# Optimization experiments

Measured on AMD Instinct MI355X. Metric: run time of the kernel, lower is better.

## Reference

```python
import jax, jax.numpy as jnp
import numpy as np

B, S, D, H, BS, L, FF, V = 2, 4096, 1024, 16, 64, 4, 4096, 50000
HD = D // H; NB = S // BS; NM = NB - 2; R = 3

def layernorm(x, g, b):
    mu = x.mean(-1, keepdims=True)
    var = ((x - mu) ** 2).mean(-1, keepdims=True)
    return (x - mu) * jax.lax.rsqrt(var + 1e-5) * g + b

def bigbird_attn(x, neg, rand_attn, Wq, bq, Wk, bk, Wv, bv, Wo, bo):
    heads = lambda t: t.reshape(B, S, H, HD).transpose(0, 2, 1, 3)
    q, k, v = heads(x @ Wq + bq), heads(x @ Wk + bk), heads(x @ Wv + bv)
    scale = np.float32(1.0 / np.sqrt(HD))
    qb = q.reshape(B, H, NB, BS, HD); kb = k.reshape(B, H, NB, BS, HD); vb = v.reshape(B, H, NB, BS, HD)
    negb = neg.reshape(B, NB, BS)
    # global query blocks (first & last) attend densely to all keys
    qg = jnp.concatenate([qb[:, :, 0], qb[:, :, -1]], axis=2)  # [B,H,2*BS,HD]
    sg = jnp.einsum('bhqd,bhkd->bhqk', qg, k) * scale + neg[:, None, None, :]
    ctx_g = jnp.einsum('bhqk,bhkd->bhqd', jax.nn.softmax(sg, -1), v)
    # middle query blocks: sliding window(3) + global(2) + random(R) key blocks
    win_k = jnp.stack([kb[:, :, i:i + NM] for i in range(3)], axis=3)  # [B,H,NM,3,BS,HD]
    win_v = jnp.stack([vb[:, :, i:i + NM] for i in range(3)], axis=3)
    gidx = jnp.array([0, NB - 1])
    g_k = jnp.broadcast_to(kb[:, :, gidx][:, :, None], (B, H, NM, 2, BS, HD))
    g_v = jnp.broadcast_to(vb[:, :, gidx][:, :, None], (B, H, NM, 2, BS, HD))
    hix = jnp.arange(H)[:, None, None]
    r_k = kb[:, hix, rand_attn]  # [B,H,NM,R,BS,HD]
    r_v = vb[:, hix, rand_attn]
    K = 3 + 2 + R
    keys = jnp.concatenate([win_k, g_k, r_k], axis=3).reshape(B, H, NM, K * BS, HD)
    vals = jnp.concatenate([win_v, g_v, r_v], axis=3).reshape(B, H, NM, K * BS, HD)
    win_m = jnp.stack([negb[:, i:i + NM] for i in range(3)], axis=2)  # [B,NM,3,BS]
    g_m = jnp.broadcast_to(negb[:, gidx][:, None], (B, NM, 2, BS))
    m_wg = jnp.concatenate([win_m, g_m], axis=2).reshape(B, 1, NM, 5 * BS)
    r_m = negb[:, rand_attn].reshape(B, H, NM, R * BS)
    m_all = jnp.concatenate([jnp.broadcast_to(m_wg, (B, H, NM, 5 * BS)), r_m], axis=-1)
    sm = jnp.einsum('bhnqd,bhnkd->bhnqk', qb[:, :, 1:-1], keys) * scale + m_all[:, :, :, None, :]
    ctx_m = jnp.einsum('bhnqk,bhnkd->bhnqd', jax.nn.softmax(sm, -1), vals)
    ctx = jnp.concatenate([ctx_g[:, :, None, :BS], ctx_m, ctx_g[:, :, None, BS:]], axis=2)
    out = ctx.reshape(B, H, S, HD).transpose(0, 2, 1, 3).reshape(B, S, D)
    return out @ Wo + bo

def reference(input_ids, attention_mask, rand_attn, emb, Wq, bq, Wk, bk, Wv, bv, Wo, bo, ln1_g, ln1_b, W1, b1, W2, b2, ln2_g, ln2_b, lnf_g, lnf_b, projW, projb):
    x = emb[input_ids]
    neg = (1.0 - attention_mask.astype(jnp.float32)) * (-1e9)
    for l in range(L):  # pre-norm transformer encoder layers
        x = x + bigbird_attn(layernorm(x, ln1_g[l], ln1_b[l]), neg, rand_attn,
                             Wq[l], bq[l], Wk[l], bk[l], Wv[l], bv[l], Wo[l], bo[l])
        h = layernorm(x, ln2_g[l], ln2_b[l])
        x = x + (jax.nn.gelu(h @ W1[l] + b1[l]) @ W2[l] + b2[l])
    x = layernorm(x, lnf_g, lnf_b)
    feats = x.mean(axis=1)  # pooled output (mean over tokens)
    feats = feats / jnp.maximum(jnp.linalg.norm(feats, axis=-1, keepdims=True), 1e-12)
    return feats @ projW + projb

def setup_inputs():
    key = jax.random.key(0)
    ks = jax.random.split(key, 16)
    init = lambda k, shp: (0.02 * jax.random.normal(k, shp)).astype(jnp.float32)
    return {
        'input_ids': jax.random.randint(ks[0], (B, S), 0, V),
        'attention_mask': jnp.ones((B, S), dtype=jnp.int32),
        'rand_attn': jax.random.randint(ks[1], (H, NM, R), 1, NB - 1),
        'emb': init(ks[2], (V, D)),
        'Wq': init(ks[3], (L, D, D)), 'bq': jnp.zeros((L, D), jnp.float32),
        'Wk': init(ks[4], (L, D, D)), 'bk': jnp.zeros((L, D), jnp.float32),
        'Wv': init(ks[5], (L, D, D)), 'bv': jnp.zeros((L, D), jnp.float32),
        'Wo': init(ks[6], (L, D, D)), 'bo': jnp.zeros((L, D), jnp.float32),
        'ln1_g': jnp.ones((L, D), jnp.float32), 'ln1_b': jnp.zeros((L, D), jnp.float32),
        'W1': init(ks[7], (L, D, FF)), 'b1': jnp.zeros((L, FF), jnp.float32),
        'W2': init(ks[8], (L, FF, D)), 'b2': jnp.zeros((L, D), jnp.float32),
        'ln2_g': jnp.ones((L, D), jnp.float32), 'ln2_b': jnp.zeros((L, D), jnp.float32),
        'lnf_g': jnp.ones((D,), jnp.float32), 'lnf_b': jnp.zeros((D,), jnp.float32),
        'projW': init(ks[9], (D, 512)), 'projb': jnp.zeros((512,), jnp.float32),
    }
```

## Files before the change

kernel.cpp:

```cpp
#include <hip/hip_runtime.h>
#include <hip/hip_bf16.h>
#include <cstdint>
#include <cstddef>

#define BATCH 2
#define SEQ   4096
#define DIM   1024
#define NHEAD 16
#define HDIM  64
#define NBLK  64
#define NMID  62
#define NRAND 3
#define NLAYER 4
#define FFDIM 4096
#define ROWS  (BATCH*SEQ)
#define KSPL  8
#define QKVLD (3*DIM)

using f32x4 = __attribute__((ext_vector_type(4))) float;
using s16x8 = __attribute__((ext_vector_type(8))) short;
using s16x4 = __attribute__((ext_vector_type(4))) short;

__device__ inline float bf2f(short s) {
    unsigned u = ((unsigned)(unsigned short)s) << 16;
    union { unsigned u; float f; } cv; cv.u = u; return cv.f;
}
__device__ inline short f2bf(float f) {
    union { float f; unsigned u; } cv; cv.f = f;
    unsigned u = cv.u;
    unsigned r = (u + 0x7fffu + ((u >> 16) & 1u)) >> 16;
    return (short)r;
}
__device__ inline float gelu_f(float x) {
    float u = 0.7978845608028654f * (x + 0.044715f * x * x * x);
    float a = fabsf(u);
    float th = 1.f - 2.f / (1.f + __expf(2.f * a));
    th = copysignf(th, u);
    return 0.5f * x * (1.f + th);
}

__device__ inline void gload16(const short* g, short* l) {
    __builtin_amdgcn_global_load_lds(
        (const __attribute__((address_space(1))) void*)g,
        (__attribute__((address_space(3))) void*)l,
        16, 0, 0);
}

__global__ __launch_bounds__(256) void embed_kernel(
    const int* __restrict__ ids, const float* __restrict__ emb, float* __restrict__ x)
{
    int row = blockIdx.x;
    int id  = ids[row];
    ((float4*)x)[(size_t)row * 256 + threadIdx.x] =
        ((const float4*)emb)[(size_t)id * 256 + threadIdx.x];
}

__global__ __launch_bounds__(256) void neg_kernel(
    const int* __restrict__ mask, float* __restrict__ neg)
{
    int i = blockIdx.x * 256 + threadIdx.x;
    if (i < ROWS) neg[i] = (1.f - (float)mask[i]) * -1e9f;
}

__global__ __launch_bounds__(256) void biaspack_kernel(
    const float* __restrict__ bq, const float* __restrict__ bk,
    const float* __restrict__ bv, float* __restrict__ b3)
{
    int i = blockIdx.x * 256 + threadIdx.x;
    float v = (i < DIM) ? bq[i] : (i < 2 * DIM) ? bk[i - DIM] : bv[i - 2 * DIM];
    b3[i] = v;
}

template<int OUTBF>
__global__ __launch_bounds__(256) void ln_kernel(
    const float* __restrict__ x, const float* __restrict__ g,
    const float* __restrict__ bia, void* __restrict__ out)
{
    __shared__ float s1[4], s2[4];
    int row = blockIdx.x, t = threadIdx.x;
    const float* xr = x + (size_t)row * DIM;
    float4 v = ((const float4*)xr)[t];
    float s = v.x + v.y + v.z + v.w;
    #pragma unroll
    for (int o = 32; o > 0; o >>= 1) s += __shfl_xor(s, o, 64);
    if ((t & 63) == 0) s1[t >> 6] = s;
    __syncthreads();
    float mu = (s1[0] + s1[1] + s1[2] + s1[3]) * (1.f / DIM);
    float dx = v.x - mu, dy = v.y - mu, dz = v.z - mu, dw = v.w - mu;
    float q = dx*dx + dy*dy + dz*dz + dw*dw;
    #pragma unroll
    for (int o = 32; o > 0; o >>= 1) q += __shfl_xor(q, o, 64);
    if ((t & 63) == 0) s2[t >> 6] = q;
    __syncthreads();
    float var = (s2[0] + s2[1] + s2[2] + s2[3]) * (1.f / DIM);
    float rs  = rsqrtf(var + 1e-5f);
    float4 gg = ((const float4*)g)[t];
    float4 bb = ((const float4*)bia)[t];
    float o0 = dx * rs * gg.x + bb.x;
    float o1 = dy * rs * gg.y + bb.y;
    float o2 = dz * rs * gg.z + bb.z;
    float o3 = dw * rs * gg.w + bb.w;
    if (OUTBF) {
        s16x4 ov = { f2bf(o0), f2bf(o1), f2bf(o2), f2bf(o3) };
        ((s16x4*)out)[(size_t)row * (DIM/4) + t] = ov;
    } else {
        float4 ov = { o0, o1, o2, o3 };
        ((float4*)out)[(size_t)row * (DIM/4) + t] = ov;
    }
}

__global__ __launch_bounds__(256) void wconv_kernel(
    const float* __restrict__ W, short* __restrict__ Wt, int K, int N)
{
    __shared__ float tile[32][33];
    int k0 = blockIdx.x * 32, n0 = blockIdx.y * 32;
    int t = threadIdx.x;
    int r = t >> 3, c = (t & 7) * 4;
    float4 v = *(const float4*)(W + (size_t)(k0 + r) * N + n0 + c);
    tile[r][c+0] = v.x; tile[r][c+1] = v.y; tile[r][c+2] = v.z; tile[r][c+3] = v.w;
    __syncthreads();
    s16x4 ov;
    #pragma unroll
    for (int jj = 0; jj < 4; ++jj) ov[jj] = f2bf(tile[c + jj][r]);
    *(s16x4*)(Wt + (size_t)(n0 + r) * K + k0 + c) = ov;
}

__global__ __launch_bounds__(256) void vtrans_kernel(
    const short* __restrict__ qkv, short* __restrict__ vT)
{
    __shared__ short tile[64][66];
    const int sb = blockIdx.x, h = blockIdx.y, b = blockIdx.z;
    const int t = threadIdx.x;
    {
        int row = t >> 2, c0 = (t & 3) * 16;
        const short* src = qkv + 2 * DIM + (size_t)(b * SEQ + sb * 64 + row) * QKVLD + h * HDIM + c0;
        s16x8 a0 = ((const s16x8*)src)[0];
        s16x8 a1 = ((const s16x8*)src)[1];
        #pragma unroll
        for (int i = 0; i < 8; ++i) { tile[row][c0 + i] = a0[i]; tile[row][c0 + 8 + i] = a1[i]; }
    }
    __syncthreads();
    {
        int d = t >> 2, k0 = (t & 3) * 16;
        s16x8 o0, o1;
        #pragma unroll
        for (int i = 0; i < 8; ++i) { o0[i] = tile[k0 + i][d]; o1[i] = tile[k0 + 8 + i][d]; }
        short* dst = vT + (size_t)((b * NHEAD + h) * HDIM + d) * SEQ + sb * 64 + k0;
        ((s16x8*)dst)[0] = o0;
        ((s16x8*)dst)[1] = o1;
    }
}

template<int EPI>
__global__ __launch_bounds__(512) void gemm256_kernel(
    const short* __restrict__ A, const short* __restrict__ Bt,
    const float* __restrict__ bias, const float* __restrict__ resid,
    void* __restrict__ Cout, int M, int N, int K, int klen)
{
    __shared__ short As[2][256 * 64];
    __shared__ short Bs[2][256 * 64];
    const int t = threadIdx.x;
    const int m0 = blockIdx.x * 256, n0 = blockIdx.y * 256;
    const int lane = t & 63, wave = t >> 6;
    const int wm = wave >> 2, wn = wave & 3;
    const int lrow = lane >> 3;
    const int lksw = ((lane & 7) ^ lrow) * 8;

    f32x4 acc[8][4];
    #pragma unroll
    for (int m = 0; m < 8; ++m)
        #pragma unroll
        for (int n = 0; n < 4; ++n)
            acc[m][n] = f32x4{0.f, 0.f, 0.f, 0.f};

    auto STAGE = [&](int side, int kt) {
        #pragma unroll
        for (int c = 0; c < 4; ++c) {
            int chunk = wave + c * 8;
            int row = chunk * 8 + lrow;
            gload16(A  + (size_t)(m0 + row) * K + kt + lksw, &As[side][chunk * 512]);
            gload16(Bt + (size_t)(n0 + row) * K + kt + lksw, &Bs[side][chunk * 512]);
        }
    };

    const int k0 = blockIdx.z * klen;
    STAGE(0, k0);
    __syncthreads();

    int cur = 0;
    for (int kt = k0; kt < k0 + klen; kt += 64) {
        if (kt + 64 < k0 + klen) STAGE(cur ^ 1, kt + 64);
        const short* Ac = As[cur];
        const short* Bc = Bs[cur];
        #pragma unroll
        for (int kk = 0; kk < 2; ++kk) {
            const int cb = kk * 64 + (lane >> 4) * 16;
            s16x8 bfr[4];
            #pragma unroll
            for (int n = 0; n < 4; ++n) {
                int rB = wn * 64 + n * 16 + (lane & 15);
                bfr[n] = *(const s16x8*)((const char*)Bc + rB * 128 + (cb ^ ((rB & 7) << 4)));
            }
            #pragma unroll
            for (int mq = 0; mq < 4; ++mq) {
                s16x8 af[2];
                #pragma unroll
                for (int i = 0; i < 2; ++i) {
                    int rA = wm * 128 + mq * 32 + i * 16 + (lane & 15);
                    af[i] = *(const s16x8*)((const char*)Ac + rA * 128 + (cb ^ ((rA & 7) << 4)));
                }
                #pragma unroll
                for (int i = 0; i < 2; ++i)
                    #pragma unroll
                    for (int n = 0; n < 4; ++n)
                        acc[mq * 2 + i][n] = __builtin_amdgcn_mfma_f32_16x16x32_bf16(
                            af[i], bfr[n], acc[mq * 2 + i][n], 0, 0, 0);
            }
        }
        __syncthreads();
        cur ^= 1;
    }

    const int rbase = m0 + wm * 128 + ((lane >> 4) << 2);
    const int cbase = n0 + wn * 64 + (lane & 15);
    #pragma unroll
    for (int m = 0; m < 8; ++m) {
        #pragma unroll
        for (int n = 0; n < 4; ++n) {
            #pragma unroll
            for (int j = 0; j < 4; ++j) {
                int row = rbase + m * 16 + j;
                int col = cbase + n * 16;
                size_t idx = (size_t)row * N + col;
                float val = acc[m][n][j];
                if (EPI == 3) {
                    ((float*)Cout)[(size_t)blockIdx.z * ((size_t)M * N) + idx] = val;
                } else {
                    val += bias[col];
                    if (EPI == 1) val = gelu_f(val);
                    ((short*)Cout)[idx] = f2bf(val);
                }
            }
        }
    }
    (void)resid;
}

template<int EPI>
__global__ __launch_bounds__(256) void gemm_kernel(
    const short* __restrict__ A, const short* __restrict__ Bt,
    const float* __restrict__ bias, const float* __restrict__ resid,
    void* __restrict__ Cout, int M, int N, int K, int klen)
{
    __shared__ short As[128 * 64];
    __shared__ short Bs[128 * 64];
    const int t = threadIdx.x;
    const int m0 = blockIdx.x * 128, n0 = blockIdx.y * 128;
    const int lane = t & 63, wave = t >> 6;
    const int wr = (wave >> 1) * 64, wc = (wave & 1) * 64;
    const int lrow = lane >> 3;
    const int lksw = ((lane & 7) ^ lrow) * 8;

    f32x4 acc[4][4];
    #pragma unroll
    for (int m = 0; m < 4; ++m)
        #pragma unroll
        for (int n = 0; n < 4; ++n)
            acc[m][n] = f32x4{0.f, 0.f, 0.f, 0.f};

    const int k0 = blockIdx.z * klen;
    for (int kt = k0; kt < k0 + klen; kt += 64) {
        #pragma unroll
        for (int c = 0; c < 4; ++c) {
            int chunk = wave * 4 + c;
            int row = chunk * 8 + lrow;
            gload16(A  + (size_t)(m0 + row) * K + kt + lksw, As + chunk * 512);
            gload16(Bt + (size_t)(n0 + row) * K + kt + lksw, Bs + chunk * 512);
        }
        asm volatile("s_waitcnt vmcnt(0)" ::: "memory");
        __syncthreads();
        #pragma unroll
        for (int kk = 0; kk < 2; ++kk) {
            s16x8 af[4], bfr[4];
            int cb = kk * 64 + (lane >> 4) * 16;
            #pragma unroll
            for (int i = 0; i < 4; ++i) {
                int rA = wr + i * 16 + (lane & 15);
                af[i]  = *(const s16x8*)((const char*)As + rA * 128 + (cb ^ ((rA & 7) << 4)));
                int rB = wc + i * 16 + (lane & 15);
                bfr[i] = *(const s16x8*)((const char*)Bs + rB * 128 + (cb ^ ((rB & 7) << 4)));
            }
            #pragma unroll
            for (int m = 0; m < 4; ++m)
                #pragma unroll
                for (int n = 0; n < 4; ++n)
                    acc[m][n] = __builtin_amdgcn_mfma_f32_16x16x32_bf16(
                        af[m], bfr[n], acc[m][n], 0, 0, 0);
        }
        __syncthreads();
    }

    const int rbase = m0 + wr + ((lane >> 4) << 2);
    const int cbase = n0 + wc + (lane & 15);
    #pragma unroll
    for (int m = 0; m < 4; ++m) {
        #pragma unroll
        for (int n = 0; n < 4; ++n) {
            #pragma unroll
            for (int j = 0; j < 4; ++j) {
                int row = rbase + m * 16 + j;
                int col = cbase + n * 16;
                size_t idx = (size_t)row * N + col;
                float val = acc[m][n][j] + bias[col];
                if (EPI == 1) val = gelu_f(val);
                if (EPI == 2) ((float*)Cout)[idx] = val + resid[idx];
                else          ((short*)Cout)[idx] = f2bf(val);
            }
        }
    }
}

__global__ __launch_bounds__(256) void kred_kernel(
    const float* __restrict__ part, const float* __restrict__ bias, float* __restrict__ x)
{
    const size_t MN = (size_t)ROWS * DIM;
    size_t idx = (size_t)blockIdx.x * DIM + threadIdx.x * 4;
    float4 p0 = *(const float4*)(part + idx);
    float4 p1 = *(const float4*)(part + MN + idx);
    float4 bb = *(const float4*)(bias + threadIdx.x * 4);
    float4 xv = *(const float4*)(x + idx);
    float4 o = { xv.x + p0.x + p1.x + bb.x,
                 xv.y + p0.y + p1.y + bb.y,
                 xv.z + p0.z + p1.z + bb.z,
                 xv.w + p0.w + p1.w + bb.w };
    *(float4*)(x + idx) = o;
}

__device__ inline void attn_tile_mfma(
    const short* __restrict__ kglob, const short* __restrict__ vtglob,
    const float* __restrict__ negp, int kld,
    short* Ks, short* Vs, float* kmask,
    const s16x8* qfrag, f32x4* o, float& mr, float& lsum)
{
    const int t = threadIdx.x;
    const int lane = t & 63;
    const int q15 = lane & 15, g = lane >> 4;
    const int sw = (lane & 7) << 4;

    {
        int row = t >> 2, c0 = (t & 3) * 16;
        int rsw = (row & 7) << 4;
        const short* ksrc = kglob + (size_t)row * kld + c0;
        s16x8 a0 = ((const s16x8*)ksrc)[0];
        s16x8 a1 = ((const s16x8*)ksrc)[1];
        char* kdst = (char*)Ks + row * 128;
        *(s16x8*)(kdst + ((c0 * 2)      ^ rsw)) = a0;
        *(s16x8*)(kdst + ((c0 * 2 + 16) ^ rsw)) = a1;
        const short* vsrc = vtglob + (size_t)row * SEQ + c0;
        s16x8 b0 = ((const s16x8*)vsrc)[0];
        s16x8 b1 = ((const s16x8*)vsrc)[1];
        char* vdst = (char*)Vs + row * 128;
        *(s16x8*)(vdst + ((c0 * 2)      ^ rsw)) = b0;
        *(s16x8*)(vdst + ((c0 * 2 + 16) ^ rsw)) = b1;
        if (t < 16) ((float4*)kmask)[t] = ((const float4*)negp)[t];
    }
    __syncthreads();

    f32x4 s[4];
    #pragma unroll
    for (int f = 0; f < 4; ++f) s[f] = f32x4{0.f, 0.f, 0.f, 0.f};
    #pragma unroll
    for (int ch = 0; ch < 2; ++ch) {
        #pragma unroll
        for (int f = 0; f < 4; ++f) {
            s16x8 kf = *(const s16x8*)((const char*)Ks + (16 * f + q15) * 128 + ((ch * 64 + g * 16) ^ sw));
            s[f] = __builtin_amdgcn_mfma_f32_16x16x32_bf16(kf, qfrag[ch], s[f], 0, 0, 0);
        }
    }

    float p[4][4];
    float mt = -1e30f;
    #pragma unroll
    for (int f = 0; f < 4; ++f) {
        float4 km = ((const float4*)kmask)[f * 4 + g];
        #pragma unroll
        for (int j = 0; j < 4; ++j) {
            float val = s[f][j] * 0.125f + ((const float*)&km)[j];
            p[f][j] = val;
            mt = fmaxf(mt, val);
        }
    }
    mt = fmaxf(mt, __shfl_xor(mt, 16, 64));
    mt = fmaxf(mt, __shfl_xor(mt, 32, 64));
    float mn = fmaxf(mr, mt);
    float psum = 0.f;
    #pragma unroll
    for (int f = 0; f < 4; ++f)
        #pragma unroll
        for (int j = 0; j < 4; ++j) {
            float e = __expf(p[f][j] - mn);
            p[f][j] = e;
            psum += e;
        }
    psum += __shfl_xor(psum, 16, 64);
    psum += __shfl_xor(psum, 32, 64);
    float fc = __expf(mr - mn);
    mr = mn;
    lsum = lsum * fc + psum;
    #pragma unroll
    for (int dt = 0; dt < 4; ++dt)
        #pragma unroll
        for (int j = 0; j < 4; ++j) o[dt][j] *= fc;

    unsigned pk[4][2];
    #pragma unroll
    for (int f = 0; f < 4; ++f)
        #pragma unroll
        for (int pp = 0; pp < 2; ++pp)
            pk[f][pp] = ((unsigned)(unsigned short)f2bf(p[f][2 * pp + 1]) << 16)
                      |  (unsigned)(unsigned short)f2bf(p[f][2 * pp]);

    const int bsel = (lane >> 4) & 1, asel = (lane >> 5) & 1;
    #pragma unroll
    for (int c = 0; c < 2; ++c) {
        union { s16x8 v; int u[4]; } pb;
        #pragma unroll
        for (int w = 0; w < 4; ++w) {
            int src = q15 + 16 * (2 * bsel + (w >> 1));
            int lo = __shfl((int)pk[2 * c][w & 1], src, 64);
            int hi = __shfl((int)pk[2 * c + 1][w & 1], src, 64);
            pb.u[w] = asel ? hi : lo;
        }
        #pragma unroll
        for (int dt = 0; dt < 4; ++dt) {
            s16x8 vf = *(const s16x8*)((const char*)Vs + (16 * dt + q15) * 128 + ((c * 64 + g * 16) ^ sw));
            o[dt] = __builtin_amdgcn_mfma_f32_16x16x32_bf16(vf, pb.v, o[dt], 0, 0, 0);
        }
    }
    __syncthreads();
}

__device__ inline void stage_q64_swz(const short* __restrict__ qglob, int qld, short* Qs)
{
    int t = threadIdx.x;
    int row = t >> 2, c0 = (t & 3) * 16;
    int rsw = (row & 7) << 4;
    const short* src = qglob + (size_t)row * qld + c0;
    s16x8 a0 = ((const s16x8*)src)[0];
    s16x8 a1 = ((const s16x8*)src)[1];
    char* dst = (char*)Qs + row * 128;
    *(s16x8*)(dst + ((c0 * 2)      ^ rsw)) = a0;
    *(s16x8*)(dst + ((c0 * 2 + 16) ^ rsw)) = a1;
}

__global__ __launch_bounds__(256) void attn_middle_mfma(
    const short* __restrict__ qkv, const short* __restrict__ vT,
    const float* __restrict__ neg, const int* __restrict__ rand_attn, short* __restrict__ ctx)
{
    __shared__ short Qs[64 * 64];
    __shared__ short Ks[64 * 64];
    __shared__ short Vs[64 * 64];
    __shared__ float kmask[64];

    const int j = blockIdx.x, h = blockIdx.y, b = blockIdx.z;
    const int n = j + 1;
    const int t = threadIdx.x;
    const int lane = t & 63, wave = t >> 6;
    const int q15 = lane & 15, g = lane >> 4;
    const int sw = (lane & 7) << 4;

    stage_q64_swz(qkv + (size_t)(b * SEQ + n * 64) * QKVLD + h * HDIM, QKVLD, Qs);
    __syncthreads();

    s16x8 qfrag[2];
    {
        int qrow = wave * 16 + q15;
        #pragma unroll
        for (int ch = 0; ch < 2; ++ch)
            qfrag[ch] = *(const s16x8*)((const char*)Qs + qrow * 128 + ((ch * 64 + g * 16) ^ sw));
    }

    int kbl[8];
    kbl[0] = n - 1; kbl[1] = n; kbl[2] = n + 1; kbl[3] = 0; kbl[4] = NBLK - 1;
    {
        const int* ra = rand_attn + ((size_t)h * NMID + j) * NRAND;
        kbl[5] = ra[0]; kbl[6] = ra[1]; kbl[7] = ra[2];
    }

    f32x4 o[4];
    #pragma unroll
    for (int dt = 0; dt < 4; ++dt) o[dt] = f32x4{0.f, 0.f, 0.f, 0.f};
    float mr = -1e30f, lsum = 0.f;

    const short* kbase  = qkv + DIM + (size_t)b * SEQ * QKVLD + h * HDIM;
    const short* vtbase = vT + (size_t)(b * NHEAD + h) * HDIM * SEQ;
    const float* negb   = neg + (size_t)b * SEQ;

    #pragma unroll 1
    for (int ib = 0; ib < 8; ++ib) {
        int kbn = kbl[ib];
        attn_tile_mfma(kbase + (size_t)kbn * 64 * QKVLD, vtbase + kbn * 64,
                       negb + kbn * 64, QKVLD, Ks, Vs, kmask, qfrag, o, mr, lsum);
    }

    float inv = 1.f / lsum;
    short* obase = ctx + (size_t)(b * SEQ + n * 64 + wave * 16 + q15) * DIM + h * HDIM;
    #pragma unroll
    for (int dt = 0; dt < 4; ++dt) {
        s16x4 ov;
        #pragma unroll
        for (int jj = 0; jj < 4; ++jj) ov[jj] = f2bf(o[dt][jj] * inv);
        *(s16x4*)(obase + dt * 16 + g * 4) = ov;
    }
}

__global__ __launch_bounds__(256) void attn_global_mfma(
    const short* __restrict__ qkv, const short* __restrict__ vT,
    const float* __restrict__ neg, float* __restrict__ part)
{
    __shared__ short Qs[64 * 64];
    __shared__ short Ks[64 * 64];
    __shared__ short Vs[64 * 64];
    __shared__ float kmask[64];

    const int qb = blockIdx.x >> 3, ks = blockIdx.x & 7;
    const int h = blockIdx.y, b = blockIdx.z;
    const int tok0 = qb ? (SEQ - 64) : 0;
    const int t = threadIdx.x;
    const int lane = t & 63, wave = t >> 6;
    const int q15 = lane & 15, g = lane >> 4;
    const int sw = (lane & 7) << 4;

    stage_q64_swz(qkv + (size_t)(b * SEQ + tok0) * QKVLD + h * HDIM, QKVLD, Qs);
    __syncthreads();

    s16x8 qfrag[2];
    {
        int qrow = wave * 16 + q15;
        #pragma unroll
        for (int ch = 0; ch < 2; ++ch)
            qfrag[ch] = *(const s16x8*)((const char*)Qs + qrow * 128 + ((ch * 64 + g * 16) ^ sw));
    }

    f32x4 o[4];
    #pragma unroll
    for (int dt = 0; dt < 4; ++dt) o[dt] = f32x4{0.f, 0.f, 0.f, 0.f};
    float mr = -1e30f, lsum = 0.f;

    const short* kbase  = qkv + DIM + (size_t)b * SEQ * QKVLD + h * HDIM;
    const short* vtbase = vT + (size_t)(b * NHEAD + h) * HDIM * SEQ;
    const float* negb   = neg + (size_t)b * SEQ;

    #pragma unroll 1
    for (int ib = 0; ib < 8; ++ib) {
        int kbn = ks * 8 + ib;
        attn_tile_mfma(kbase + (size_t)kbn * 64 * QKVLD, vtbase + kbn * 64,
                       negb + kbn * 64, QKVLD, Ks, Vs, kmask, qfrag, o, mr, lsum);
    }

    float* pbase = part + ((size_t)(((b * NHEAD + h) * 2 + qb) * KSPL + ks)) * 4224;
    int qrow = wave * 16 + q15;
    #pragma unroll
    for (int dt = 0; dt < 4; ++dt)
        *(f32x4*)(pbase + qrow * 64 + dt * 16 + g * 4) = o[dt];
    if (g == 0) { pbase[4096 + qrow] = mr; pbase[4160 + qrow] = lsum; }
}

__global__ __launch_bounds__(256) void attn_greduce(
    const float* __restrict__ part, short* __restrict__ ctx)
{
    const int qb = blockIdx.x, h = blockIdx.y, b = blockIdx.z;
    const int tok0 = qb ? (SEQ - 64) : 0;
    const int t = threadIdx.x;
    const int qq = t >> 2, d0 = (t & 3) * 16;
    const float* base = part + ((size_t)(((b * NHEAD + h) * 2 + qb) * KSPL)) * 4224;

    float m = -1e30f;
    #pragma unroll 1
    for (int s = 0; s < KSPL; ++s)
        m = fmaxf(m, base[(size_t)s * 4224 + 4096 + qq]);
    float L = 0.f;
    float acc[16];
    #pragma unroll
    for (int i = 0; i < 16; ++i) acc[i] = 0.f;
    #pragma unroll 1
    for (int s = 0; s < KSPL; ++s) {
        const float* bp = base + (size_t)s * 4224;
        float w = __expf(bp[4096 + qq] - m);
        L += w * bp[4160 + qq];
        const float4* row = (const float4*)(bp + qq * 64 + d0);
        #pragma unroll
        for (int v4 = 0; v4 < 4; ++v4) {
            float4 val = row[v4];
            acc[v4 * 4 + 0] = fmaf(w, val.x, acc[v4 * 4 + 0]);
            acc[v4 * 4 + 1] = fmaf(w, val.y, acc[v4 * 4 + 1]);
            acc[v4 * 4 + 2] = fmaf(w, val.z, acc[v4 * 4 + 2]);
            acc[v4 * 4 + 3] = fmaf(w, val.w, acc[v4 * 4 + 3]);
        }
    }
    float inv = 1.f / L;
    short* dst = ctx + (size_t)(b * SEQ + tok0 + qq) * DIM + h * HDIM + d0;
    s16x8 o0, o1;
    #pragma unroll
    for (int i = 0; i < 8; ++i) { o0[i] = f2bf(acc[i] * inv); o1[i] = f2bf(acc[8 + i] * inv); }
    ((s16x8*)dst)[0] = o0;
    ((s16x8*)dst)[1] = o1;
}

__global__ __launch_bounds__(256) void colsum1_kernel(
    const float* __restrict__ xln, float* __restrict__ partial)
{
    const int ch = blockIdx.x, b = blockIdx.y, t = threadIdx.x;
    const float* base = xln + ((size_t)b * SEQ + ch * 32) * DIM + t * 4;
    float4 acc = {0.f, 0.f, 0.f, 0.f};
    #pragma unroll 4
    for (int r = 0; r < 32; ++r) {
        float4 v = *(const float4*)(base + (size_t)r * DIM);
        acc.x += v.x; acc.y += v.y; acc.z += v.z; acc.w += v.w;
    }
    *(float4*)(partial + ((size_t)(b * 128 + ch)) * DIM + t * 4) = acc;
}

__global__ __launch_bounds__(256) void colsum2_kernel(
    const float* __restrict__ partial, float* __restrict__ feats)
{
    const int b = blockIdx.x, t = threadIdx.x;
    float4 acc = {0.f, 0.f, 0.f, 0.f};
    #pragma unroll 1
    for (int ch = 0; ch < 128; ++ch) {
        float4 v = *(const float4*)(partial + ((size_t)(b * 128 + ch)) * DIM + t * 4);
        acc.x += v.x; acc.y += v.y; acc.z += v.z; acc.w += v.w;
    }
    const float is = 1.f / SEQ;
    float4 o = { acc.x * is, acc.y * is, acc.z * is, acc.w * is };
    *(float4*)(feats + (size_t)b * DIM + t * 4) = o;
}

__global__ __launch_bounds__(256) void head_kernel(
    const float* __restrict__ feats, const float* __restrict__ projW,
    const float* __restrict__ projb, float* __restrict__ out)
{
    __shared__ float f[DIM];
    __shared__ float slots[4];
    int b = blockIdx.x, t = threadIdx.x;
    float ss = 0.f;
    for (int i = t; i < DIM; i += 256) {
        float vv = feats[b * DIM + i];
        f[i] = vv;
        ss += vv * vv;
    }
    #pragma unroll
    for (int o = 32; o > 0; o >>= 1) ss += __shfl_xor(ss, o, 64);
    if ((t & 63) == 0) slots[t >> 6] = ss;
    __syncthreads();
    float nrm = sqrtf(slots[0] + slots[1] + slots[2] + slots[3]);
    float inv = 1.f / fmaxf(nrm, 1e-12f);
    for (int o = t; o < 512; o += 256) {
        float acc = 0.f;
        for (int d = 0; d < DIM; ++d)
            acc = fmaf(f[d], projW[(size_t)d * 512 + o], acc);
        out[b * 512 + o] = acc * inv + projb[o];
    }
}

extern "C" void kernel_launch(void* const* d_in, const int* in_sizes, int n_in,
                              void* d_out, int out_size, void* d_ws, size_t ws_size,
                              hipStream_t stream)
{
    (void)in_sizes; (void)n_in; (void)out_size; (void)ws_size;
    const int*   ids   = (const int*)d_in[0];
    const int*   amask = (const int*)d_in[1];
    const int*   rnd   = (const int*)d_in[2];
    const float* emb   = (const float*)d_in[3];
    const float* Wq    = (const float*)d_in[4];
    const float* bq    = (const float*)d_in[5];
    const float* Wk    = (const float*)d_in[6];
    const float* bk    = (const float*)d_in[7];
    const float* Wv    = (const float*)d_in[8];
    const float* bv    = (const float*)d_in[9];
    const float* Wo    = (const float*)d_in[10];
    const float* bo    = (const float*)d_in[11];
    const float* ln1g  = (const float*)d_in[12];
    const float* ln1b  = (const float*)d_in[13];
    const float* W1    = (const float*)d_in[14];
    const float* b1    = (const float*)d_in[15];
    const float* W2    = (const float*)d_in[16];
    const float* b2    = (const float*)d_in[17];
    const float* ln2g  = (const float*)d_in[18];
    const float* ln2b  = (const float*)d_in[19];
    const float* lnfg  = (const float*)d_in[20];
    const float* lnfb  = (const float*)d_in[21];
    const float* projW = (const float*)d_in[22];
    const float* projb = (const float*)d_in[23];
    float* out = (float*)d_out;

    char* ws = (char*)d_ws;
    size_t off = 0;
    float* x    = (float*)(ws + off); off += (size_t)ROWS * DIM * 4;
    float* xn_f = (float*)(ws + off);
    short* xn_b = (short*)(ws + off); off += (size_t)ROWS * DIM * 4;
    short* qkv  = (short*)(ws + off); off += (size_t)ROWS * QKVLD * 2;
    short* vT   = (short*)(ws + off); off += (size_t)ROWS * DIM * 2;
    short* ctxb = (short*)(ws + off); off += (size_t)ROWS * DIM * 2;
    short* ffb  = (short*)(ws + off); off += (size_t)ROWS * FFDIM * 2;
    short* wt   = (short*)(ws + off); off += (size_t)FFDIM * DIM * 2;
    float* neg  = (float*)(ws + off); off += (size_t)ROWS * 4;
    float* bias3= (float*)(ws + off); off += (size_t)QKVLD * 4;
    float* feats= (float*)(ws + off); off += (size_t)BATCH * DIM * 4;
    float* part = (float*)(ws + off); off += (size_t)BATCH * NHEAD * 2 * KSPL * 4224 * 4;
    float* cpart= (float*)(ws + off); off += (size_t)BATCH * 128 * DIM * 4;
    float* ff2p = (float*)qkv;

    embed_kernel<<<ROWS, 256, 0, stream>>>(ids, emb, x);
    neg_kernel<<<(ROWS + 255) / 256, 256, 0, stream>>>(amask, neg);

    for (int l = 0; l < NLAYER; ++l) {
        ln_kernel<1><<<ROWS, 256, 0, stream>>>(x, ln1g + l * DIM, ln1b + l * DIM, xn_b);

        wconv_kernel<<<dim3(DIM/32, DIM/32), 256, 0, stream>>>(Wq + (size_t)l*DIM*DIM, wt,               DIM, DIM);
        wconv_kernel<<<dim3(DIM/32, DIM/32), 256, 0, stream>>>(Wk + (size_t)l*DIM*DIM, wt + 1024*1024,   DIM, DIM);
        wconv_kernel<<<dim3(DIM/32, DIM/32), 256, 0, stream>>>(Wv + (size_t)l*DIM*DIM, wt + 2*1024*1024, DIM, DIM);
        biaspack_kernel<<<QKVLD/256, 256, 0, stream>>>(bq + l*DIM, bk + l*DIM, bv + l*DIM, bias3);
        gemm256_kernel<0><<<dim3(ROWS/256, QKVLD/256), 512, 0, stream>>>(xn_b, wt, bias3, nullptr, qkv, ROWS, QKVLD, DIM, DIM);

        vtrans_kernel<<<dim3(SEQ/64, NHEAD, BATCH), 256, 0, stream>>>(qkv, vT);

        attn_global_mfma<<<dim3(2 * KSPL, NHEAD, BATCH), 256, 0, stream>>>(qkv, vT, neg, part);
        attn_middle_mfma<<<dim3(NMID, NHEAD, BATCH), 256, 0, stream>>>(qkv, vT, neg, rnd, ctxb);
        attn_greduce<<<dim3(2, NHEAD, BATCH), 256, 0, stream>>>(part, ctxb);

        wconv_kernel<<<dim3(DIM/32, DIM/32), 256, 0, stream>>>(Wo + (size_t)l*DIM*DIM, wt, DIM, DIM);
        gemm_kernel<2><<<dim3(ROWS/128, DIM/128), 256, 0, stream>>>(ctxb, wt, bo + l*DIM, x, x, ROWS, DIM, DIM, DIM);

        ln_kernel<1><<<ROWS, 256, 0, stream>>>(x, ln2g + l * DIM, ln2b + l * DIM, xn_b);

        wconv_kernel<<<dim3(DIM/32, FFDIM/32), 256, 0, stream>>>(W1 + (size_t)l*DIM*FFDIM, wt, DIM, FFDIM);
        gemm256_kernel<1><<<dim3(ROWS/256, FFDIM/256), 512, 0, stream>>>(xn_b, wt, b1 + l*FFDIM, nullptr, ffb, ROWS, FFDIM, DIM, DIM);
        wconv_kernel<<<dim3(FFDIM/32, DIM/32), 256, 0, stream>>>(W2 + (size_t)l*FFDIM*DIM, wt, FFDIM, DIM);
        gemm256_kernel<3><<<dim3(ROWS/256, DIM/256, 2), 512, 0, stream>>>(ffb, wt, nullptr, nullptr, ff2p, ROWS, DIM, FFDIM, FFDIM/2);
        kred_kernel<<<ROWS, 256, 0, stream>>>(ff2p, b2 + l*DIM, x);
    }

    ln_kernel<0><<<ROWS, 256, 0, stream>>>(x, lnfg, lnfb, xn_f);
    colsum1_kernel<<<dim3(SEQ/32, BATCH), 256, 0, stream>>>(xn_f, cpart);
    colsum2_kernel<<<BATCH, 256, 0, stream>>>(cpart, feats);
    head_kernel<<<BATCH, 256, 0, stream>>>(feats, projW, projb, out);
}
```

Measured before the change: 1.774 ms.

## Restructure 256x256 GEMM main loop into four barrier-separated MFMA phases with split staging

The 256-tile GEMM main loop is rewritten into four quadrant phases. Each phase reads A/B fragments from LDS, then issues the A or B global prefetch for the next k-tile, then runs MFMAs under raised s_setprio between raw s_barriers. The staging layout is changed so each wave loads the rows it will later consume, and an explicit vmcnt wait replaces the end-of-iteration syncthreads. Separately, all weight conversions are hoisted out of the layer loop into per-layer buffers, which uses more workspace but removes the per-layer serialization of conversion kernels. The barrier choreography risks stalls or hazards if the ordering is subtly wrong.

```diff
diff --git a/kernel.cpp b/kernel.cpp
--- a/kernel.cpp
+++ b/kernel.cpp
@@ -16,6 +16,7 @@
 #define ROWS  (BATCH*SEQ)
 #define KSPL  8
 #define QKVLD (3*DIM)
+#define WLAYER (12*1024*1024)
 
 using f32x4 = __attribute__((ext_vector_type(4))) float;
 using s16x8 = __attribute__((ext_vector_type(8))) short;
@@ -163,8 +164,11 @@
     const int m0 = blockIdx.x * 256, n0 = blockIdx.y * 256;
     const int lane = t & 63, wave = t >> 6;
     const int wm = wave >> 2, wn = wave & 3;
+    const int l15 = lane & 15;
     const int lrow = lane >> 3;
     const int lksw = ((lane & 7) ^ lrow) * 8;
+    const int ga = wn;
+    const int hb = wn >> 1, gb = wm * 2 + (wn & 1);
 
     f32x4 acc[8][4];
     #pragma unroll
@@ -173,56 +177,110 @@
         for (int n = 0; n < 4; ++n)
             acc[m][n] = f32x4{0.f, 0.f, 0.f, 0.f};
 
-    auto STAGE = [&](int side, int kt) {
+    auto STAGE_A = [&](int side, int kt) {
         #pragma unroll
         for (int c = 0; c < 4; ++c) {
-            int chunk = wave + c * 8;
-            int row = chunk * 8 + lrow;
-            gload16(A  + (size_t)(m0 + row) * K + kt + lksw, &As[side][chunk * 512]);
-            gload16(Bt + (size_t)(n0 + row) * K + kt + lksw, &Bs[side][chunk * 512]);
+            int row = wm * 128 + c * 32 + ga * 8 + lrow;
+            gload16(A + (size_t)(m0 + row) * K + kt + lksw,
+                    &As[side][wm * 8192 + c * 2048 + ga * 512]);
         }
     };
-
-    const int k0 = blockIdx.z * klen;
-    STAGE(0, k0);
+    auto STAGE_B = [&](int side, int kt) {
+        #pragma unroll
+        for (int c = 0; c < 4; ++c) {
+            int row = hb * 128 + c * 32 + gb * 8 + lrow;
+            gload16(Bt + (size_t)(n0 + row) * K + kt + lksw,
+                    &Bs[side][hb * 8192 + c * 2048 + gb * 512]);
+        }
+    };
+    auto RD_A = [&](const short* buf, int mf, int kk) -> s16x8 {
+        int r = wm * 128 + mf * 16 + l15;
+        int cb = kk * 64 + (lane >> 4) * 16;
+        return *(const s16x8*)((const char*)buf + r * 128 + (cb ^ ((r & 7) << 4)));
+    };
+    auto RD_B = [&](const short* buf, int nf, int kk) -> s16x8 {
+        int r = wn * 64 + nf * 16 + l15;
+        int cb = kk * 64 + (lane >> 4) * 16;
+        return *(const s16x8*)((const char*)buf + r * 128 + (cb ^ ((r & 7) << 4)));
+    };
+
+    const int k0 = blockIdx.z * klen, kend = k0 + klen;
+    STAGE_A(0, k0);
+    STAGE_B(0, k0);
+    asm volatile("s_waitcnt vmcnt(0)" ::: "memory");
     __syncthreads();
 
     int cur = 0;
-    for (int kt = k0; kt < k0 + klen; kt += 64) {
-        if (kt + 64 < k0 + klen) STAGE(cur ^ 1, kt + 64);
+    for (int kt = k0; kt < kend; kt += 64) {
         const short* Ac = As[cur];
         const short* Bc = Bs[cur];
-        #pragma unroll
-        for (int kk = 0; kk < 2; ++kk) {
-            const int cb = kk * 64 + (lane >> 4) * 16;
-            s16x8 bfr[4];
+        const bool nxt = (kt + 64 < kend);
+        s16x8 af[4][2], bf[2][2], bf2[2][2];
+
+        #pragma unroll
+        for (int mf = 0; mf < 4; ++mf) { af[mf][0] = RD_A(Ac, mf, 0); af[mf][1] = RD_A(Ac, mf, 1); }
+        #pragma unroll
+        for (int nf = 0; nf < 2; ++nf) { bf[nf][0] = RD_B(Bc, nf, 0); bf[nf][1] = RD_B(Bc, nf, 1); }
+        if (nxt) STAGE_A(cur ^ 1, kt + 64);
+        __builtin_amdgcn_s_barrier();
+        __builtin_amdgcn_s_setprio(1);
+        #pragma unroll
+        for (int kk = 0; kk < 2; ++kk)
             #pragma unroll
-            for (int n = 0; n < 4; ++n) {
-                int rB = wn * 64 + n * 16 + (lane & 15);
-                bfr[n] = *(const s16x8*)((const char*)Bc + rB * 128 + (cb ^ ((rB & 7) << 4)));
-            }
+            for (int mf = 0; mf < 4; ++mf)
+                #pragma unroll
+                for (int nf = 0; nf < 2; ++nf)
+                    acc[mf][nf] = __builtin_amdgcn_mfma_f32_16x16x32_bf16(af[mf][kk], bf[nf][kk], acc[mf][nf], 0, 0, 0);
+        __builtin_amdgcn_s_setprio(0);
+        __builtin_amdgcn_s_barrier();
+
+        #pragma unroll
+        for (int nf = 0; nf < 2; ++nf) { bf2[nf][0] = RD_B(Bc, 2 + nf, 0); bf2[nf][1] = RD_B(Bc, 2 + nf, 1); }
+        if (nxt) STAGE_B(cur ^ 1, kt + 64);
+        __builtin_amdgcn_s_barrier();
+        __builtin_amdgcn_s_setprio(1);
+        #pragma unroll
+        for (int kk = 0; kk < 2; ++kk)
             #pragma unroll
-            for (int mq = 0; mq < 4; ++mq) {
-                s16x8 af[2];
+            for (int mf = 0; mf < 4; ++mf)
                 #pragma unroll
-                for (int i = 0; i < 2; ++i) {
-                    int rA = wm * 128 + mq * 32 + i * 16 + (lane & 15);
-                    af[i] = *(const s16x8*)((const char*)Ac + rA * 128 + (cb ^ ((rA & 7) << 4)));
-                }
+                for (int nf = 0; nf < 2; ++nf)
+                    acc[mf][2 + nf] = __builtin_amdgcn_mfma_f32_16x16x32_bf16(af[mf][kk], bf2[nf][kk], acc[mf][2 + nf], 0, 0, 0);
+        __builtin_amdgcn_s_setprio(0);
+        __builtin_amdgcn_s_barrier();
+
+        #pragma unroll
+        for (int mf = 0; mf < 4; ++mf) { af[mf][0] = RD_A(Ac, 4 + mf, 0); af[mf][1] = RD_A(Ac, 4 + mf, 1); }
+        __builtin_amdgcn_s_barrier();
+        __builtin_amdgcn_s_setprio(1);
+        #pragma unroll
+        for (int kk = 0; kk < 2; ++kk)
+            #pragma unroll
+            for (int mf = 0; mf < 4; ++mf)
                 #pragma unroll
-                for (int i = 0; i < 2; ++i)
-                    #pragma unroll
-                    for (int n = 0; n < 4; ++n)
-                        acc[mq * 2 + i][n] = __builtin_amdgcn_mfma_f32_16x16x32_bf16(
-                            af[i], bfr[n], acc[mq * 2 + i][n], 0, 0, 0);
-            }
-        }
-        __syncthreads();
+                for (int nf = 0; nf < 2; ++nf)
+                    acc[4 + mf][nf] = __builtin_amdgcn_mfma_f32_16x16x32_bf16(af[mf][kk], bf[nf][kk], acc[4 + mf][nf], 0, 0, 0);
+        __builtin_amdgcn_s_setprio(0);
+        __builtin_amdgcn_s_barrier();
+
+        asm volatile("s_waitcnt vmcnt(0)" ::: "memory");
+        __builtin_amdgcn_s_barrier();
+        __builtin_amdgcn_s_setprio(1);
+        #pragma unroll
+        for (int kk = 0; kk < 2; ++kk)
+            #pragma unroll
+            for (int mf = 0; mf < 4; ++mf)
+                #pragma unroll
+                for (int nf = 0; nf < 2; ++nf)
+                    acc[4 + mf][2 + nf] = __builtin_amdgcn_mfma_f32_16x16x32_bf16(af[mf][kk], bf2[nf][kk], acc[4 + mf][2 + nf], 0, 0, 0);
+        __builtin_amdgcn_s_setprio(0);
+        __builtin_amdgcn_s_barrier();
+
         cur ^= 1;
     }
 
     const int rbase = m0 + wm * 128 + ((lane >> 4) << 2);
-    const int cbase = n0 + wn * 64 + (lane & 15);
+    const int cbase = n0 + wn * 64 + l15;
     #pragma unroll
     for (int m = 0; m < 8; ++m) {
         #pragma unroll
@@ -703,9 +761,9 @@
     short* vT   = (short*)(ws + off); off += (size_t)ROWS * DIM * 2;
     short* ctxb = (short*)(ws + off); off += (size_t)ROWS * DIM * 2;
     short* ffb  = (short*)(ws + off); off += (size_t)ROWS * FFDIM * 2;
-    short* wt   = (short*)(ws + off); off += (size_t)FFDIM * DIM * 2;
+    short* wt4  = (short*)(ws + off); off += (size_t)NLAYER * WLAYER * 2;
     float* neg  = (float*)(ws + off); off += (size_t)ROWS * 4;
-    float* bias3= (float*)(ws + off); off += (size_t)QKVLD * 4;
+    float* bias3= (float*)(ws + off); off += (size_t)NLAYER * QKVLD * 4;
     float* feats= (float*)(ws + off); off += (size_t)BATCH * DIM * 4;
     float* part = (float*)(ws + off); off += (size_t)BATCH * NHEAD * 2 * KSPL * 4224 * 4;
     float* cpart= (float*)(ws + off); off += (size_t)BATCH * 128 * DIM * 4;
@@ -715,13 +773,28 @@
     neg_kernel<<<(ROWS + 255) / 256, 256, 0, stream>>>(amask, neg);
 
     for (int l = 0; l < NLAYER; ++l) {
+        short* wq3 = wt4 + (size_t)l * WLAYER;
+        short* wo  = wq3 + 3 * 1024 * 1024;
+        short* w1t = wo  + 1024 * 1024;
+        short* w2t = w1t + 4 * 1024 * 1024;
+        wconv_kernel<<<dim3(DIM/32, DIM/32), 256, 0, stream>>>(Wq + (size_t)l*DIM*DIM, wq3,               DIM, DIM);
+        wconv_kernel<<<dim3(DIM/32, DIM/32), 256, 0, stream>>>(Wk + (size_t)l*DIM*DIM, wq3 + 1024*1024,   DIM, DIM);
+        wconv_kernel<<<dim3(DIM/32, DIM/32), 256, 0, stream>>>(Wv + (size_t)l*DIM*DIM, wq3 + 2*1024*1024, DIM, DIM);
+        wconv_kernel<<<dim3(DIM/32, DIM/32), 256, 0, stream>>>(Wo + (size_t)l*DIM*DIM, wo, DIM, DIM);
+        wconv_kernel<<<dim3(DIM/32, FFDIM/32), 256, 0, stream>>>(W1 + (size_t)l*DIM*FFDIM, w1t, DIM, FFDIM);
+        wconv_kernel<<<dim3(FFDIM/32, DIM/32), 256, 0, stream>>>(W2 + (size_t)l*FFDIM*DIM, w2t, FFDIM, DIM);
+        biaspack_kernel<<<QKVLD/256, 256, 0, stream>>>(bq + l*DIM, bk + l*DIM, bv + l*DIM, bias3 + (size_t)l*QKVLD);
+    }
+
+    for (int l = 0; l < NLAYER; ++l) {
+        short* wq3 = wt4 + (size_t)l * WLAYER;
+        short* wo  = wq3 + 3 * 1024 * 1024;
+        short* w1t = wo  + 1024 * 1024;
+        short* w2t = w1t + 4 * 1024 * 1024;
+
         ln_kernel<1><<<ROWS, 256, 0, stream>>>(x, ln1g + l * DIM, ln1b + l * DIM, xn_b);
 
-        wconv_kernel<<<dim3(DIM/32, DIM/32), 256, 0, stream>>>(Wq + (size_t)l*DIM*DIM, wt,               DIM, DIM);
-        wconv_kernel<<<dim3(DIM/32, DIM/32), 256, 0, stream>>>(Wk + (size_t)l*DIM*DIM, wt + 1024*1024,   DIM, DIM);
-        wconv_kernel<<<dim3(DIM/32, DIM/32), 256, 0, stream>>>(Wv + (size_t)l*DIM*DIM, wt + 2*1024*1024, DIM, DIM);
-        biaspack_kernel<<<QKVLD/256, 256, 0, stream>>>(bq + l*DIM, bk + l*DIM, bv + l*DIM, bias3);
-        gemm256_kernel<0><<<dim3(ROWS/256, QKVLD/256), 512, 0, stream>>>(xn_b, wt, bias3, nullptr, qkv, ROWS, QKVLD, DIM, DIM);
+        gemm256_kernel<0><<<dim3(ROWS/256, QKVLD/256), 512, 0, stream>>>(xn_b, wq3, bias3 + (size_t)l*QKVLD, nullptr, qkv, ROWS, QKVLD, DIM, DIM);
 
         vtrans_kernel<<<dim3(SEQ/64, NHEAD, BATCH), 256, 0, stream>>>(qkv, vT);
 
@@ -729,15 +802,12 @@
         attn_middle_mfma<<<dim3(NMID, NHEAD, BATCH), 256, 0, stream>>>(qkv, vT, neg, rnd, ctxb);
         attn_greduce<<<dim3(2, NHEAD, BATCH), 256, 0, stream>>>(part, ctxb);
 
-        wconv_kernel<<<dim3(DIM/32, DIM/32), 256, 0, stream>>>(Wo + (size_t)l*DIM*DIM, wt, DIM, DIM);
-        gemm_kernel<2><<<dim3(ROWS/128, DIM/128), 256, 0, stream>>>(ctxb, wt, bo + l*DIM, x, x, ROWS, DIM, DIM, DIM);
+        gemm_kernel<2><<<dim3(ROWS/128, DIM/128), 256, 0, stream>>>(ctxb, wo, bo + l*DIM, x, x, ROWS, DIM, DIM, DIM);
 
         ln_kernel<1><<<ROWS, 256, 0, stream>>>(x, ln2g + l * DIM, ln2b + l * DIM, xn_b);
 
-        wconv_kernel<<<dim3(DIM/32, FFDIM/32), 256, 0, stream>>>(W1 + (size_t)l*DIM*FFDIM, wt, DIM, FFDIM);
-        gemm256_kernel<1><<<dim3(ROWS/256, FFDIM/256), 512, 0, stream>>>(xn_b, wt, b1 + l*FFDIM, nullptr, ffb, ROWS, FFDIM, DIM, DIM);
-        wconv_kernel<<<dim3(FFDIM/32, DIM/32), 256, 0, stream>>>(W2 + (size_t)l*FFDIM*DIM, wt, FFDIM, DIM);
-        gemm256_kernel<3><<<dim3(ROWS/256, DIM/256, 2), 512, 0, stream>>>(ffb, wt, nullptr, nullptr, ff2p, ROWS, DIM, FFDIM, FFDIM/2);
+        gemm256_kernel<1><<<dim3(ROWS/256, FFDIM/256), 512, 0, stream>>>(xn_b, w1t, b1 + l*FFDIM, nullptr, ffb, ROWS, FFDIM, DIM, DIM);
+        gemm256_kernel<3><<<dim3(ROWS/256, DIM/256, 2), 512, 0, stream>>>(ffb, w2t, nullptr, nullptr, ff2p, ROWS, DIM, FFDIM, FFDIM/2);
         kred_kernel<<<ROWS, 256, 0, stream>>>(ff2p, b2 + l*DIM, x);
     }
 
```

Result: no change. 1.792 ms (+1.0%).
